# Performance work log

Hardware: AMD Instinct MI355X
Metric: run time of the kernel (lower is better)

## Reference

```python
import jax, jax.numpy as jnp
import numpy as np

V, E, SH, H = 10004, 300, 1024, 512
B, T = 128, 50
PAD = 10003


def setup_inputs() -> dict:
    key = jax.random.key(0)
    ks = jax.random.split(key, 13)
    s = 0.05
    emb = s * jax.random.normal(ks[0], (V, E), dtype=jnp.float32)
    emb = emb.at[PAD].set(0.0)  # padding_idx row is zero
    G = 2 * H  # GRU hidden size is 2*hid_size
    Wih = s * jax.random.normal(ks[1], (3 * G, E), dtype=jnp.float32)
    Whh = s * jax.random.normal(ks[2], (3 * G, G), dtype=jnp.float32)
    bih = s * jax.random.normal(ks[3], (3 * G,), dtype=jnp.float32)
    bhh = s * jax.random.normal(ks[4], (3 * G,), dtype=jnp.float32)
    W1 = s * jax.random.normal(ks[5], (H, SH), dtype=jnp.float32)
    b1 = s * jax.random.normal(ks[6], (H,), dtype=jnp.float32)
    W2 = s * jax.random.normal(ks[7], (E, G), dtype=jnp.float32)
    b2 = s * jax.random.normal(ks[8], (E,), dtype=jnp.float32)
    Wout = s * jax.random.normal(ks[9], (V, E), dtype=jnp.float32)
    ses_encoding = jax.random.normal(ks[10], (1, B, SH), dtype=jnp.float32)
    x = jax.random.randint(ks[11], (B, T), 0, 10000)
    return {"ses_encoding": ses_encoding, "x": x, "emb": emb, "Wih": Wih,
            "Whh": Whh, "bih": bih, "bhh": bhh, "W1": W1, "b1": b1,
            "W2": W2, "b2": b2, "Wout": Wout}


def reference(ses_encoding, x, emb, Wih, Whh, bih, bhh, W1, b1, W2, b2, Wout):
    hid = W1.shape[0]            # hid_size
    G = Whh.shape[1]             # 2*hid_size (GRU hidden)
    # ses_encoding = tanh(lin1(ses_encoding)), then viewed to [1, B, hid]
    ses = jnp.tanh(jnp.einsum('lbs,hs->lbh', ses_encoding, W1) + b1)[0]  # [B, hid]
    emb_all = emb[x]             # [B, T, E] (dropout inactive at eval)

    def step(h, e_t):
        # GRU hidden input each step: concat(prev_half, ses) -> [B, 2*hid]
        Hfull = jnp.concatenate([h, ses], axis=-1)
        gx = e_t @ Wih.T + bih                      # [B, 3G]
        gh = Hfull @ Whh.T + bhh                    # [B, 3G]
        r = jax.nn.sigmoid(gx[:, :G] + gh[:, :G])
        z = jax.nn.sigmoid(gx[:, G:2 * G] + gh[:, G:2 * G])
        n = jnp.tanh(gx[:, 2 * G:] + r * gh[:, 2 * G:])
        hnew = (1.0 - z) * n + z * Hfull            # [B, 2*hid]
        o = hnew @ W2.T + b2 + e_t                  # lin2(hid_o) + residual emb
        logits = o @ Wout.T                         # [B, V]
        return hnew[:, :hid], logits

    _, logits = jax.lax.scan(step, ses, jnp.swapaxes(emb_all, 0, 1))
    return jnp.swapaxes(logits, 0, 1)               # [B, T, V]
```

## Files before the change

### kernel.cpp

```cpp
#include <hip/hip_runtime.h>


typedef __bf16 bf16x8 __attribute__((ext_vector_type(8)));
typedef float f32x4 __attribute__((ext_vector_type(4)));
typedef unsigned long long u64;

#define SENT 0xFFC1FFC1FFC1FFC1ull

__global__ void cvt_kernel(const float* __restrict__ src, int srows, int scols,
                           int sstride, int soff,
                           __bf16* __restrict__ dst, int drows, int dcols) {
    int idx = blockIdx.x * 256 + threadIdx.x;
    int total = drows * dcols;
    if (idx >= total) return;
    int r = idx / dcols, c = idx % dcols;
    float v = 0.0f;
    if (r < srows && c < scols) v = src[(size_t)r * sstride + soff + c];
    dst[idx] = (__bf16)v;
}

__global__ void emb_kernel(const int* __restrict__ x, const float* __restrict__ emb,
                           __bf16* __restrict__ embbf) {
    int m = blockIdx.x;
    int t = m >> 7, b = m & 127;
    int tok = x[b * 50 + t];
    const float* src = emb + (size_t)tok * 300;
    for (int i = threadIdx.x; i < 320; i += 64) {
        float v = (i < 300) ? src[i] : 0.0f;
        embbf[(size_t)m * 320 + i] = (__bf16)v;
    }
}

__global__ void prefill_kernel(u64* __restrict__ F) {
    size_t idx = (size_t)blockIdx.x * 256 + threadIdx.x;
    size_t row = idx >> 7, off = idx & 127;
    __hip_atomic_store(F + (128 + row) * 256 + off, SENT,
                       __ATOMIC_RELAXED, __HIP_MEMORY_SCOPE_AGENT);
}

struct GemmParams {
    const __bf16* A; int lda;
    const __bf16* B; int ldb; int Brows;
    int K;
    const float* bias;
    float* outF; int ldo; int Nstore;
    __bf16* outBf;
    const __bf16* res;
    const float* add2;
    int ld2; int add2lim;
};

template <int EPI>
__launch_bounds__(256, 2)
__global__ void gemm_bt(GemmParams p) {
    __shared__ __bf16 As[128][40];
    __shared__ __bf16 Bs[128][40];

    const int tid = threadIdx.x;
    const int lane = tid & 63;
    const int wid = tid >> 6;
    const int wr = wid >> 1, wc = wid & 1;
    const int m0 = blockIdx.x * 128, c0 = blockIdx.y * 128;
    const int lrow = lane & 15;
    const int kq = lane >> 4;

    f32x4 acc[4][4];
#pragma unroll
    for (int i = 0; i < 4; ++i)
#pragma unroll
        for (int j = 0; j < 4; ++j) acc[i][j] = (f32x4){0.f, 0.f, 0.f, 0.f};

    for (int kb = 0; kb < p.K; kb += 32) {
#pragma unroll
        for (int i = 0; i < 2; ++i) {
            int chunk = i * 256 + tid;
            int row = chunk >> 2;
            int cc = (chunk & 3) * 8;
            bf16x8 va = *reinterpret_cast<const bf16x8*>(
                p.A + (size_t)(m0 + row) * p.lda + kb + cc);
            *reinterpret_cast<bf16x8*>(&As[row][cc]) = va;
            bf16x8 vb;
#pragma unroll
            for (int q = 0; q < 8; ++q) vb[q] = (__bf16)0.0f;
            int grow = c0 + row;
            if (grow < p.Brows)
                vb = *reinterpret_cast<const bf16x8*>(
                    p.B + (size_t)grow * p.ldb + kb + cc);
            *reinterpret_cast<bf16x8*>(&Bs[row][cc]) = vb;
        }
        __syncthreads();

        bf16x8 af[4], bfr[4];
#pragma unroll
        for (int m = 0; m < 4; ++m)
            af[m] = *reinterpret_cast<const bf16x8*>(&As[wr * 64 + m * 16 + lrow][kq * 8]);
#pragma unroll
        for (int n = 0; n < 4; ++n)
            bfr[n] = *reinterpret_cast<const bf16x8*>(&Bs[wc * 64 + n * 16 + lrow][kq * 8]);
#pragma unroll
        for (int m = 0; m < 4; ++m)
#pragma unroll
            for (int n = 0; n < 4; ++n)
                acc[m][n] = __builtin_amdgcn_mfma_f32_16x16x32_bf16(
                    af[m], bfr[n], acc[m][n], 0, 0, 0);
        __syncthreads();
    }

#pragma unroll
    for (int m = 0; m < 4; ++m) {
#pragma unroll
        for (int n = 0; n < 4; ++n) {
#pragma unroll
            for (int i = 0; i < 4; ++i) {
                int r = m0 + wr * 64 + m * 16 + kq * 4 + i;
                int c = c0 + wc * 64 + n * 16 + lrow;
                float v = acc[m][n][i];
                if constexpr (EPI == 1) {
                    v = tanhf(v + p.bias[c]);
                    p.outBf[(size_t)r * p.ldo + c] = (__bf16)v;
                    p.outF[(size_t)c * 128 + r] = v;
                } else if constexpr (EPI == 2) {
                    int ro = (r & 127) * 50 + (r >> 7);
                    if (c < 300) {
                        v += p.bias[c] + (float)p.res[(size_t)r * 320 + c];
                        p.outBf[(size_t)ro * 320 + c] = (__bf16)v;
                    } else if (c < 320) {
                        p.outBf[(size_t)ro * 320 + c] = (__bf16)0.0f;
                    }
                } else if constexpr (EPI == 3) {
                    if (c < p.Nstore) p.outF[(size_t)r * p.ldo + c] = v;
                } else {
                    if (c < p.Brows) {
                        float v2 = v + p.bias[r];
                        if (p.add2 && r < p.add2lim)
                            v2 += p.add2[(size_t)r * 128 + (c & 127)];
                        p.outF[(size_t)(c >> 7) * p.ldo + (size_t)r * 128 + (c & 127)] = v2;
                    }
                }
            }
        }
    }
}

#define SCAN_NB 64
__launch_bounds__(256, 1)
__global__ void scan_kernel(const __bf16* __restrict__ Whh_a,
                            const float* __restrict__ gxT,
                            const float* __restrict__ ghcT,
                            const float* __restrict__ sesT,
                            u64* __restrict__ F) {
    __shared__ char Ws[98304];
    const int tid = threadIdx.x;
    const int lane = tid & 63;
    const int wid = tid >> 6;
    const int wr = wid >> 1, wc = wid & 1;
    const int bid = blockIdx.x;
    const int q = bid >> 4;
    const int j0 = (bid & 15) * 32;
    const int lrow = lane & 15, kq = lane >> 4;

    for (int it = 0; it < 24; ++it) {
        int c = it * 256 + tid;
        int rl = c >> 6, o16 = c & 63;
        int g = rl >> 5, jj = rl & 31;
        bf16x8 v = *reinterpret_cast<const bf16x8*>(
            Whh_a + (size_t)(g * 1024 + j0 + jj) * 512 + o16 * 8);
        *reinterpret_cast<bf16x8*>(Ws + rl * 1024 + ((o16 * 16) ^ ((rl & 7) << 4))) = v;
    }

    const int b_g = q * 32 + wc * 16 + lrow;
    const int jbase = j0 + wr * 16 + kq * 4;

    float cn[4], hprev[4], gcur[12], gpre[12];
#pragma unroll
    for (int i = 0; i < 4; ++i) {
        cn[i] = ghcT[(size_t)(2048 + jbase + i) * 128 + b_g];
        hprev[i] = sesT[(size_t)(jbase + i) * 128 + b_g];
    }
#pragma unroll
    for (int i = 0; i < 4; ++i) {
        gpre[i]     = gxT[(size_t)(jbase + i) * 128 + b_g];
        gpre[4 + i] = gxT[(size_t)(1024 + jbase + i) * 128 + b_g];
        gpre[8 + i] = gxT[(size_t)(2048 + jbase + i) * 128 + b_g];
    }

    __syncthreads();

    for (int t = 0; t < 50; ++t) {
#pragma unroll
        for (int i = 0; i < 12; ++i) gcur[i] = gpre[i];
        {
            int tn = (t < 49) ? t + 1 : 49;
            const float* gxt = gxT + (size_t)tn * 3072 * 128;
#pragma unroll
            for (int i = 0; i < 4; ++i) {
                gpre[i]     = gxt[(size_t)(jbase + i) * 128 + b_g];
                gpre[4 + i] = gxt[(size_t)(1024 + jbase + i) * 128 + b_g];
                gpre[8 + i] = gxt[(size_t)(2048 + jbase + i) * 128 + b_g];
            }
        }

        const u64* rowp = F + ((size_t)t * 128 + b_g) * 256 + kq * 2;
        u64 hv[32];
        for (;;) {
            bool ok = true;
#pragma unroll
            for (int kb = 0; kb < 16; ++kb) {
                u64 a = __hip_atomic_load(rowp + kb * 8,
                                          __ATOMIC_RELAXED, __HIP_MEMORY_SCOPE_AGENT);
                u64 b = __hip_atomic_load(rowp + kb * 8 + 1,
                                          __ATOMIC_RELAXED, __HIP_MEMORY_SCOPE_AGENT);
                hv[2 * kb] = a;
                hv[2 * kb + 1] = b;
                ok &= (a != SENT) & (b != SENT);
            }
            if (__all(ok)) break;
            __builtin_amdgcn_s_sleep(1);
        }

        f32x4 acc[3];
#pragma unroll
        for (int g = 0; g < 3; ++g) acc[g] = (f32x4){0.f, 0.f, 0.f, 0.f};
        const int arow0 = wr * 16 + lrow;
#pragma unroll
        for (int kb = 0; kb < 16; ++kb) {
            union { u64 u[2]; bf16x8 v; } hf;
            hf.u[0] = hv[2 * kb];
            hf.u[1] = hv[2 * kb + 1];
            int ko = kb * 64 + kq * 16;
#pragma unroll
            for (int g = 0; g < 3; ++g) {
                int arow = g * 32 + arow0;
                bf16x8 wfrag = *reinterpret_cast<const bf16x8*>(
                    Ws + arow * 1024 + (ko ^ ((arow & 7) << 4)));
                acc[g] = __builtin_amdgcn_mfma_f32_16x16x32_bf16(
                    wfrag, hf.v, acc[g], 0, 0, 0);
            }
        }

        union { u64 u; __bf16 h[4]; } pk;
#pragma unroll
        for (int i = 0; i < 4; ++i) {
            float r = 1.0f / (1.0f + expf(-(gcur[i] + acc[0][i])));
            float z = 1.0f / (1.0f + expf(-(gcur[4 + i] + acc[1][i])));
            float nn = tanhf(gcur[8 + i] + r * (acc[2][i] + cn[i]));
            float hn = (1.0f - z) * nn + z * hprev[i];
            hprev[i] = hn;
            pk.h[i] = (__bf16)hn;
        }
        __hip_atomic_store(
            F + ((size_t)(t + 1) * 128 + b_g) * 256 + (jbase >> 2), pk.u,
            __ATOMIC_RELAXED, __HIP_MEMORY_SCOPE_AGENT);
    }
}

__launch_bounds__(256, 1)
__global__ void tail_kernel(const __bf16* __restrict__ Whh_a,
                            const float* __restrict__ gxT,
                            const float* __restrict__ ghcT,
                            const float* __restrict__ sesT,
                            __bf16* __restrict__ F) {
    __shared__ char smem[131072];
    char* Ws = smem;
    char* Hs = smem + 98304;
    const int tid = threadIdx.x;
    const int lane = tid & 63;
    const int wid = tid >> 6;
    const int wr = wid >> 1, wc = wid & 1;
    const int bid = blockIdx.x;
    const int tg = bid >> 6;
    const int rem = bid & 63;
    const int q = rem >> 4;
    const int j0 = 512 + (rem & 15) * 32;
    const int lrow = lane & 15, kq = lane >> 4;

    for (int it = 0; it < 24; ++it) {
        int c = it * 256 + tid;
        int rl = c >> 6, o16 = c & 63;
        int g = rl >> 5, jj = rl & 31;
        bf16x8 v = *reinterpret_cast<const bf16x8*>(
            Whh_a + (size_t)(g * 1024 + j0 + jj) * 512 + o16 * 8);
        *reinterpret_cast<bf16x8*>(Ws + rl * 1024 + ((o16 * 16) ^ ((rl & 7) << 4))) = v;
    }

    const int b_g = q * 32 + wc * 16 + lrow;
    const int jbase = j0 + wr * 16 + kq * 4;

    float cn[4], sv[4];
#pragma unroll
    for (int i = 0; i < 4; ++i) {
        cn[i] = ghcT[(size_t)(2048 + jbase + i) * 128 + b_g];
        sv[i] = sesT[(size_t)(jbase + i - 512) * 128 + b_g];
    }

    for (int tt = tg * 10; tt < tg * 10 + 10; ++tt) {
        for (int it = 0; it < 8; ++it) {
            int c = it * 256 + tid;
            int rl = c >> 6, o16 = c & 63;
            bf16x8 v = *reinterpret_cast<const bf16x8*>(
                F + ((size_t)tt * 128 + q * 32 + rl) * 1024 + o16 * 8);
            *reinterpret_cast<bf16x8*>(Hs + rl * 1024 + ((o16 * 16) ^ ((rl & 7) << 4))) = v;
        }
        const float* gxt = gxT + (size_t)tt * 3072 * 128;
        float g0[12];
#pragma unroll
        for (int i = 0; i < 4; ++i) {
            g0[i]     = gxt[(size_t)(jbase + i) * 128 + b_g];
            g0[4 + i] = gxt[(size_t)(1024 + jbase + i) * 128 + b_g];
            g0[8 + i] = gxt[(size_t)(2048 + jbase + i) * 128 + b_g];
        }
        __syncthreads();

        f32x4 acc[3];
#pragma unroll
        for (int g = 0; g < 3; ++g) acc[g] = (f32x4){0.f, 0.f, 0.f, 0.f};
        const int hrow = wc * 16 + lrow;
        const int arow0 = wr * 16 + lrow;
        for (int kb = 0; kb < 16; ++kb) {
            int ko = kb * 64 + kq * 16;
            bf16x8 hfrag = *reinterpret_cast<const bf16x8*>(
                Hs + hrow * 1024 + (ko ^ ((hrow & 7) << 4)));
#pragma unroll
            for (int g = 0; g < 3; ++g) {
                int arow = g * 32 + arow0;
                bf16x8 wfrag = *reinterpret_cast<const bf16x8*>(
                    Ws + arow * 1024 + (ko ^ ((arow & 7) << 4)));
                acc[g] = __builtin_amdgcn_mfma_f32_16x16x32_bf16(
                    wfrag, hfrag, acc[g], 0, 0, 0);
            }
        }

        union { u64 u; __bf16 h[4]; } pk;
#pragma unroll
        for (int i = 0; i < 4; ++i) {
            float r = 1.0f / (1.0f + expf(-(g0[i] + acc[0][i])));
            float z = 1.0f / (1.0f + expf(-(g0[4 + i] + acc[1][i])));
            float nn = tanhf(g0[8 + i] + r * (acc[2][i] + cn[i]));
            pk.h[i] = (__bf16)((1.0f - z) * nn + z * sv[i]);
        }
        *reinterpret_cast<u64*>(F + ((size_t)(tt + 1) * 128 + b_g) * 1024 + jbase) = pk.u;
        __syncthreads();
    }
}

extern "C" void kernel_launch(void* const* d_in, const int* in_sizes, int n_in,
                              void* d_out, int out_size, void* d_ws, size_t ws_size,
                              hipStream_t stream) {
    const float* ses_enc = (const float*)d_in[0];
    const int*   x       = (const int*)d_in[1];
    const float* emb     = (const float*)d_in[2];
    const float* Wih     = (const float*)d_in[3];
    const float* Whh     = (const float*)d_in[4];
    const float* bih     = (const float*)d_in[5];
    const float* bhh     = (const float*)d_in[6];
    const float* W1      = (const float*)d_in[7];
    const float* b1      = (const float*)d_in[8];
    const float* W2      = (const float*)d_in[9];
    const float* b2      = (const float*)d_in[10];
    const float* Wout    = (const float*)d_in[11];
    float* out = (float*)d_out;

    char* ws = (char*)d_ws;
    float*  sesT      = (float*)(ws + 0);
    float*  ghcT      = (float*)(ws + 262144);
    __bf16* o_bf      = (__bf16*)(ws + 1835008);
    __bf16* W1_bf     = (__bf16*)(ws + 5931008);
    __bf16* Whh_a_bf  = (__bf16*)(ws + 6979584);
    __bf16* Whh_b_bf  = (__bf16*)(ws + 10125312);
    __bf16* Wih_bf    = (__bf16*)(ws + 13271040);
    __bf16* W2_bf     = (__bf16*)(ws + 15237120);
    __bf16* Wout_bf   = (__bf16*)(ws + 15851520);
    __bf16* sesenc_bf = (__bf16*)(ws + 22323200);

    char* ob = (char*)d_out;
    float*  gxT     = (float*)ob;
    __bf16* emb_bf  = (__bf16*)(ob + 80000000);
    __bf16* F       = (__bf16*)(ob + 88000000);

    dim3 blk(256);
    auto cvt = [&](const float* src, int sr, int sc, int ss, int so,
                   __bf16* dst, int dr, int dc) {
        int total = dr * dc;
        cvt_kernel<<<(total + 255) / 256, 256, 0, stream>>>(src, sr, sc, ss, so, dst, dr, dc);
    };
    cvt(W1,      512, 1024, 1024, 0,   W1_bf,     512, 1024);
    cvt(Whh,    3072,  512, 1024, 0,   Whh_a_bf, 3072,  512);
    cvt(Whh,    3072,  512, 1024, 512, Whh_b_bf, 3072,  512);
    cvt(Wih,    3072,  300,  300, 0,   Wih_bf,   3072,  320);
    cvt(W2,      300, 1024, 1024, 0,   W2_bf,     300, 1024);
    cvt(Wout,  10004,  300,  300, 0,   Wout_bf, 10112,  320);
    cvt(ses_enc, 128, 1024, 1024, 0,   sesenc_bf, 128, 1024);
    emb_kernel<<<6400, 64, 0, stream>>>(x, emb, emb_bf);
    prefill_kernel<<<3200, 256, 0, stream>>>((u64*)F);

    GemmParams P;

    P = {sesenc_bf, 1024, W1_bf, 1024, 512, 1024, b1, sesT, 1024, 512, F,
         nullptr, nullptr, 0, 0};
    gemm_bt<1><<<dim3(1, 4), blk, 0, stream>>>(P);

    P = {Whh_b_bf, 512, F, 1024, 128, 512, bhh, ghcT, 0, 0, nullptr,
         nullptr, nullptr, 0, 0};
    gemm_bt<4><<<dim3(24, 1), blk, 0, stream>>>(P);

    P = {Wih_bf, 320, emb_bf, 320, 6400, 320, bih, gxT, 3072 * 128, 0, nullptr,
         nullptr, ghcT, 0, 2048};
    gemm_bt<4><<<dim3(24, 50), blk, 0, stream>>>(P);

    scan_kernel<<<SCAN_NB, 256, 0, stream>>>(
        Whh_a_bf, gxT, ghcT, sesT, (u64*)F);

    tail_kernel<<<320, 256, 0, stream>>>(Whh_a_bf, gxT, ghcT, sesT, F);

    P = {F + 128 * 1024, 1024, W2_bf, 1024, 300, 1024, b2, nullptr, 0, 300, o_bf,
         emb_bf, nullptr, 0, 0};
    gemm_bt<2><<<dim3(50, 3), blk, 0, stream>>>(P);

    P = {o_bf, 320, Wout_bf, 320, 10112, 320, nullptr, out, 10004, 10004, nullptr,
         nullptr, nullptr, 0, 0};
    gemm_bt<3><<<dim3(50, 79), blk, 0, stream>>>(P);

    (void)in_sizes; (void)n_in; (void)out_size; (void)ws_size;
}
```

Baseline: 753.1 us.

## Replace sentinel polling on hidden state with per-wave flag array synchronization

The recurrent scan kernel stops spinning on the full hidden-state row until no sentinel values remain. Instead, each wave publishes a per-step flag after draining its stores, and consumers spin on one 64-entry flag vector per batch group before reading the hidden state once. The sentinel prefill kernel is replaced by a memset of a small flag buffer, and the next-step gx prefetch moves to after the store so it overlaps the wait. This relies on relaxed ordering plus s_waitcnt for visibility, which carries a memory-ordering risk, and the wait loop no longer sleeps.

```diff
diff --git a/kernel.cpp b/kernel.cpp
--- a/kernel.cpp
+++ b/kernel.cpp
@@ -4,8 +4,6 @@
 typedef __bf16 bf16x8 __attribute__((ext_vector_type(8)));
 typedef float f32x4 __attribute__((ext_vector_type(4)));
 typedef unsigned long long u64;
-
-#define SENT 0xFFC1FFC1FFC1FFC1ull
 
 __global__ void cvt_kernel(const float* __restrict__ src, int srows, int scols,
                            int sstride, int soff,
@@ -29,13 +27,6 @@
         float v = (i < 300) ? src[i] : 0.0f;
         embbf[(size_t)m * 320 + i] = (__bf16)v;
     }
-}
-
-__global__ void prefill_kernel(u64* __restrict__ F) {
-    size_t idx = (size_t)blockIdx.x * 256 + threadIdx.x;
-    size_t row = idx >> 7, off = idx & 127;
-    __hip_atomic_store(F + (128 + row) * 256 + off, SENT,
-                       __ATOMIC_RELAXED, __HIP_MEMORY_SCOPE_AGENT);
 }
 
 struct GemmParams {
@@ -148,7 +139,8 @@
                             const float* __restrict__ gxT,
                             const float* __restrict__ ghcT,
                             const float* __restrict__ sesT,
-                            u64* __restrict__ F) {
+                            u64* __restrict__ F,
+                            unsigned* __restrict__ flags) {
     __shared__ char Ws[98304];
     const int tid = threadIdx.x;
     const int lane = tid & 63;
@@ -187,35 +179,26 @@
     __syncthreads();
 
     for (int t = 0; t < 50; ++t) {
+        if (t > 0) {
+            const unsigned* fl = flags + ((t * 4 + q) << 6);
+            for (;;) {
+                unsigned v = __hip_atomic_load(fl + lane, __ATOMIC_RELAXED,
+                                               __HIP_MEMORY_SCOPE_AGENT);
+                if (__all(v != 0)) break;
+            }
+        }
+
 #pragma unroll
         for (int i = 0; i < 12; ++i) gcur[i] = gpre[i];
-        {
-            int tn = (t < 49) ? t + 1 : 49;
-            const float* gxt = gxT + (size_t)tn * 3072 * 128;
-#pragma unroll
-            for (int i = 0; i < 4; ++i) {
-                gpre[i]     = gxt[(size_t)(jbase + i) * 128 + b_g];
-                gpre[4 + i] = gxt[(size_t)(1024 + jbase + i) * 128 + b_g];
-                gpre[8 + i] = gxt[(size_t)(2048 + jbase + i) * 128 + b_g];
-            }
-        }
 
         const u64* rowp = F + ((size_t)t * 128 + b_g) * 256 + kq * 2;
         u64 hv[32];
-        for (;;) {
-            bool ok = true;
-#pragma unroll
-            for (int kb = 0; kb < 16; ++kb) {
-                u64 a = __hip_atomic_load(rowp + kb * 8,
-                                          __ATOMIC_RELAXED, __HIP_MEMORY_SCOPE_AGENT);
-                u64 b = __hip_atomic_load(rowp + kb * 8 + 1,
-                                          __ATOMIC_RELAXED, __HIP_MEMORY_SCOPE_AGENT);
-                hv[2 * kb] = a;
-                hv[2 * kb + 1] = b;
-                ok &= (a != SENT) & (b != SENT);
-            }
-            if (__all(ok)) break;
-            __builtin_amdgcn_s_sleep(1);
+#pragma unroll
+        for (int kb = 0; kb < 16; ++kb) {
+            hv[2 * kb]     = __hip_atomic_load(rowp + kb * 8,
+                                               __ATOMIC_RELAXED, __HIP_MEMORY_SCOPE_AGENT);
+            hv[2 * kb + 1] = __hip_atomic_load(rowp + kb * 8 + 1,
+                                               __ATOMIC_RELAXED, __HIP_MEMORY_SCOPE_AGENT);
         }
 
         f32x4 acc[3];
@@ -251,6 +234,25 @@
         __hip_atomic_store(
             F + ((size_t)(t + 1) * 128 + b_g) * 256 + (jbase >> 2), pk.u,
             __ATOMIC_RELAXED, __HIP_MEMORY_SCOPE_AGENT);
+
+        if (t < 49) {
+            asm volatile("s_waitcnt vmcnt(0)" ::: "memory");
+            if (lane == 0)
+                __hip_atomic_store(
+                    flags + (((t + 1) * 4 + q) << 6) + (bid & 15) * 4 + wid, 1u,
+                    __ATOMIC_RELAXED, __HIP_MEMORY_SCOPE_AGENT);
+        }
+
+        {
+            int tn = (t < 49) ? t + 1 : 49;
+            const float* gxt = gxT + (size_t)tn * 3072 * 128;
+#pragma unroll
+            for (int i = 0; i < 4; ++i) {
+                gpre[i]     = gxt[(size_t)(jbase + i) * 128 + b_g];
+                gpre[4 + i] = gxt[(size_t)(1024 + jbase + i) * 128 + b_g];
+                gpre[8 + i] = gxt[(size_t)(2048 + jbase + i) * 128 + b_g];
+            }
+        }
     }
 }
 
@@ -371,6 +373,7 @@
     __bf16* W2_bf     = (__bf16*)(ws + 15237120);
     __bf16* Wout_bf   = (__bf16*)(ws + 15851520);
     __bf16* sesenc_bf = (__bf16*)(ws + 22323200);
+    unsigned* flags   = (unsigned*)(ws + 22585344);
 
     char* ob = (char*)d_out;
     float*  gxT     = (float*)ob;
@@ -391,7 +394,7 @@
     cvt(Wout,  10004,  300,  300, 0,   Wout_bf, 10112,  320);
     cvt(ses_enc, 128, 1024, 1024, 0,   sesenc_bf, 128, 1024);
     emb_kernel<<<6400, 64, 0, stream>>>(x, emb, emb_bf);
-    prefill_kernel<<<3200, 256, 0, stream>>>((u64*)F);
+    hipMemsetAsync(flags, 0, 51200, stream);
 
     GemmParams P;
 
@@ -408,7 +411,7 @@
     gemm_bt<4><<<dim3(24, 50), blk, 0, stream>>>(P);
 
     scan_kernel<<<SCAN_NB, 256, 0, stream>>>(
-        Whh_a_bf, gxT, ghcT, sesT, (u64*)F);
+        Whh_a_bf, gxT, ghcT, sesT, (u64*)F, flags);
 
     tail_kernel<<<320, 256, 0, stream>>>(Whh_a_bf, gxT, ghcT, sesT, F);
 
```

Result: no change. 751.9 us (-0.2%).
